# Kernel optimization log

Measured on AMD Instinct MI355X. Metric: run time of the kernel, lower is better.

The kernel has to match this reference:

```python
import jax, jax.numpy as jnp
import numpy as np

S, V, T = 128, 64, 128
N_RBF, CUTOFF = 16, 6.0
N_ATOM, N_PROT, N_FRAG, N_BATCH = 8192, 16384, 1024, 8
K, R, EPS = 32, 3.0, 1e-4
ES_DIM = N_RBF + S + S + T  # 400
HID = 256
GATE = S + 2 * V  # 256


def rbf_encode(d):
    mu = jnp.linspace(0.0, CUTOFF, N_RBF)
    gamma = N_RBF / CUTOFF
    return jnp.exp(-jnp.square(gamma * (d[..., None] - mu)))


def tp_conv(hs, hv, src, dst, diff, es, valid, n_dst, W1, b1, W2, b2, Ws, Wv):
    """Gather -> edge-scalar-gated tensor product -> scatter-add (EquivariantTPConv)."""
    w = jax.nn.silu(es @ W1 + b1) @ W2 + b2                      # [E, S+2V] edge gates
    unit = diff / (jnp.linalg.norm(diff, axis=-1, keepdims=True) + 1e-8)
    xs = hs[src] @ Ws                                            # [E, S]
    xv = jnp.einsum('evc,vw->ewc', hv[src], Wv)                  # [E, V, 3]
    ms = jnp.where(valid[:, None], w[:, :S] * xs, 0.0)
    mv = jnp.where(valid[:, None, None],
                   w[:, S:S + V, None] * xv + w[:, S + V:, None] * unit[:, None, :], 0.0)
    agg_s = jax.ops.segment_sum(ms, dst, num_segments=n_dst)
    agg_v = jax.ops.segment_sum(mv.reshape(-1, V * 3), dst, num_segments=n_dst).reshape(n_dst, V, 3)
    return agg_s, agg_v


def fragment_inertia(local_pos, fragment_id):
    r2 = jnp.sum(local_pos * local_pos, axis=-1)
    eye = jnp.eye(3, dtype=local_pos.dtype)
    I_atom = r2[:, None, None] * eye - local_pos[:, :, None] * local_pos[:, None, :]
    I_frag = jax.ops.segment_sum(I_atom.reshape(-1, 9), fragment_id, num_segments=N_FRAG).reshape(N_FRAG, 3, 3)
    trace = jnp.trace(I_frag, axis1=-2, axis2=-1)[:, None, None]
    return I_frag + EPS * jnp.maximum(trace, 1.0) * eye


def _forward(atom_pos, prot_pos, local_pos, h_atom_s, h_atom_v, h_prot_s, h_prot_v,
             h_frag_s, h_frag_v, t_emb_atom,
             W1_ra, b1_ra, W2_ra, b2_ra, Ws_ra, Wv_ra,
             W1_af, b1_af, W2_af, b2_af, Ws_af, Wv_af,
             Wo_s, Wo_v, Wf_s, Wf_v,
             fragment_id, atom_batch, prot_batch):
    # ---- bipartite radius graph prot -> atom via masked cdist + topk ----
    d2 = (jnp.sum(atom_pos * atom_pos, -1)[:, None]
          + jnp.sum(prot_pos * prot_pos, -1)[None, :]
          - 2.0 * atom_pos @ prot_pos.T)
    dist = jnp.sqrt(jnp.maximum(d2, 0.0))                        # [N_ATOM, N_PROT]
    mask = (dist <= R) & (atom_batch[:, None] == prot_batch[None, :])
    dinf = jnp.where(mask, dist, jnp.inf)
    neg_top, src = jax.lax.top_k(-dinf, K)                       # K nearest per atom
    valid = jnp.isfinite(neg_top).reshape(-1)
    src = src.reshape(-1)
    dst = jnp.repeat(jnp.arange(N_ATOM), K)
    # ---- residue->atom TP conv ----
    diff_ra = atom_pos[dst] - prot_pos[src]
    dist_ra = jnp.linalg.norm(diff_ra, axis=-1)
    ra_es = jnp.concatenate([rbf_encode(dist_ra), h_prot_s[src], h_atom_s[dst], t_emb_atom[dst]], -1)
    ms, mv = tp_conv(h_prot_s, h_prot_v, src, dst, diff_ra, ra_es, valid, N_ATOM,
                     W1_ra, b1_ra, W2_ra, b2_ra, Ws_ra, Wv_ra)
    ha_s = h_atom_s + jax.nn.silu(ms @ Wo_s)
    ha_v = h_atom_v + jnp.einsum('nvc,vw->nwc', mv, Wo_v)
    # ---- fragment centers + atom->frag re-lift TP conv ----
    ones = jnp.ones((N_ATOM,), atom_pos.dtype)
    cnt = jnp.maximum(jax.ops.segment_sum(ones, fragment_id, num_segments=N_FRAG), 1.0)
    T_frag = jax.ops.segment_sum(atom_pos, fragment_id, num_segments=N_FRAG) / cnt[:, None]
    r_af = atom_pos - T_frag[fragment_id]
    af_es = jnp.concatenate([rbf_encode(jnp.linalg.norm(r_af, axis=-1)), ha_s,
                             h_frag_s[fragment_id], t_emb_atom], -1)
    af_valid = jnp.ones((N_ATOM,), bool)
    fs, fv = tp_conv(ha_s, ha_v, jnp.arange(N_ATOM), fragment_id, r_af, af_es, af_valid, N_FRAG,
                     W1_af, b1_af, W2_af, b2_af, Ws_af, Wv_af)
    hf_s = h_frag_s + jax.nn.silu(fs @ Wf_s)
    hf_v = h_frag_v + jnp.einsum('nvc,vw->nwc', fv, Wf_v)
    I_frag = fragment_inertia(local_pos, fragment_id)
    # single packed output [N_ATOM, 2*(S+3V)+9]; frag quantities gathered per atom
    return jnp.concatenate([ha_s, ha_v.reshape(N_ATOM, -1),
                            hf_s[fragment_id], hf_v.reshape(N_FRAG, -1)[fragment_id],
                            I_frag.reshape(N_FRAG, 9)[fragment_id]], -1)


def setup_inputs() -> dict:
    key = jax.random.key(0)
    ks = jax.random.split(key, 32)
    def w(k, shape, fan_in):
        return jax.random.normal(k, shape, jnp.float32) / np.sqrt(fan_in).astype(np.float32)
    return dict(
        atom_pos=jax.random.normal(ks[0], (N_ATOM, 3), jnp.float32),
        prot_pos=jax.random.normal(ks[1], (N_PROT, 3), jnp.float32),
        local_pos=jax.random.normal(ks[2], (N_ATOM, 3), jnp.float32),
        h_atom_s=jax.random.normal(ks[3], (N_ATOM, S), jnp.float32),
        h_atom_v=jax.random.normal(ks[4], (N_ATOM, V, 3), jnp.float32),
        h_prot_s=jax.random.normal(ks[5], (N_PROT, S), jnp.float32),
        h_prot_v=jax.random.normal(ks[6], (N_PROT, V, 3), jnp.float32),
        h_frag_s=jax.random.normal(ks[7], (N_FRAG, S), jnp.float32),
        h_frag_v=jax.random.normal(ks[8], (N_FRAG, V, 3), jnp.float32),
        t_emb_atom=jax.random.normal(ks[9], (N_ATOM, T), jnp.float32),
        W1_ra=w(ks[10], (ES_DIM, HID), ES_DIM), b1_ra=jnp.zeros((HID,), jnp.float32),
        W2_ra=w(ks[11], (HID, GATE), HID), b2_ra=jnp.zeros((GATE,), jnp.float32),
        Ws_ra=w(ks[12], (S, S), S), Wv_ra=w(ks[13], (V, V), V),
        W1_af=w(ks[14], (ES_DIM, HID), ES_DIM), b1_af=jnp.zeros((HID,), jnp.float32),
        W2_af=w(ks[15], (HID, GATE), HID), b2_af=jnp.zeros((GATE,), jnp.float32),
        Ws_af=w(ks[16], (S, S), S), Wv_af=w(ks[17], (V, V), V),
        Wo_s=w(ks[18], (S, S), S), Wo_v=w(ks[19], (V, V), V),
        Wf_s=w(ks[20], (S, S), S), Wf_v=w(ks[21], (V, V), V),
        fragment_id=jax.random.randint(ks[22], (N_ATOM,), 0, N_FRAG),
        atom_batch=jnp.sort(jax.random.randint(ks[23], (N_ATOM,), 0, N_BATCH)),
        prot_batch=jnp.sort(jax.random.randint(ks[24], (N_PROT,), 0, N_BATCH)),
    )


def reference(atom_pos, prot_pos, local_pos, h_atom_s, h_atom_v, h_prot_s, h_prot_v,
              h_frag_s, h_frag_v, t_emb_atom,
              W1_ra, b1_ra, W2_ra, b2_ra, Ws_ra, Wv_ra,
              W1_af, b1_af, W2_af, b2_af, Ws_af, Wv_af,
              Wo_s, Wo_v, Wf_s, Wf_v,
              fragment_id, atom_batch, prot_batch):
    return _forward(atom_pos, prot_pos, local_pos, h_atom_s, h_atom_v, h_prot_s, h_prot_v,
                    h_frag_s, h_frag_v, t_emb_atom,
                    W1_ra, b1_ra, W2_ra, b2_ra, Ws_ra, Wv_ra,
                    W1_af, b1_af, W2_af, b2_af, Ws_af, Wv_af,
                    Wo_s, Wo_v, Wf_s, Wf_v,
                    fragment_id, atom_batch, prot_batch)
```

## Files before the change

### kernel.cpp

```cpp
#include <hip/hip_runtime.h>
#include <hip/hip_bf16.h>

#define N_ATOM 8192
#define N_PROT 16384
#define N_FRAG 1024
#define KNN    32
#define OUTC   649

typedef __attribute__((ext_vector_type(8))) short bf16x8;
typedef __attribute__((ext_vector_type(4))) float f32x4;

__device__ __forceinline__ float silu_f(float x){ return x / (1.f + __expf(-x)); }
__device__ __forceinline__ unsigned long long ullmin2(unsigned long long a, unsigned long long b){ return a < b ? a : b; }

__device__ __forceinline__ short f2bf(float x){
    __hip_bfloat16 h = __float2bfloat16(x);
    return *reinterpret_cast<short*>(&h);
}
__device__ __forceinline__ unsigned f2bf2(float lo, float hi){
    __hip_bfloat162 h2;
    h2.x = __float2bfloat16(lo);
    h2.y = __float2bfloat16(hi);
    return *reinterpret_cast<unsigned*>(&h2);
}
__device__ __forceinline__ float bf2f(short s){
    return __uint_as_float(((unsigned)(unsigned short)s) << 16);
}

__global__ void k_ranges(const int* __restrict__ pbatch, int* __restrict__ pstart){
    int b = threadIdx.x;
    if (b <= 8){
        int lo = 0, hi = N_PROT;
        while (lo < hi){ int mid = (lo + hi) >> 1; if (pbatch[mid] < b) lo = mid + 1; else hi = mid; }
        pstart[b] = lo;
    }
}

__global__ __launch_bounds__(256) void k_knn(const float* __restrict__ apos,
                                             const float* __restrict__ ppos,
                                             const int* __restrict__ abatch,
                                             const int* __restrict__ pstart,
                                             int* __restrict__ src_out){
    __shared__ int h1[256];
    __shared__ int h2[256];
    __shared__ int s_info[6];
    __shared__ int s_nsel;
    __shared__ int s_nbound;
    __shared__ unsigned long long s_bound[192];

    const int i = blockIdx.x, t = threadIdx.x;
    const int lane = t & 63;
    const int b = abatch[i];
    const int p0 = pstart[b], p1 = pstart[b+1];
    const float ax = apos[i*3+0], ay = apos[i*3+1], az = apos[i*3+2];
    const float a2 = ax*ax + ay*ay + az*az;

    unsigned kb[12];
    int jj[12];
#pragma unroll
    for (int q = 0; q < 12; ++q){
        int j = p0 + q*256 + t;
        unsigned kk = 0xFFFFFFFFu;
        if (j < p1){
            float px = ppos[j*3+0], py = ppos[j*3+1], pz = ppos[j*3+2];
            float p2 = px*px + py*py + pz*pz;
            float dt = ax*px + ay*py + az*pz;
            float d2 = (a2 + p2) - 2.0f*dt;
            float dist = sqrtf(fmaxf(d2, 0.f));
            if (dist <= 3.0f) kk = __float_as_uint(dist);
        }
        kb[q] = kk; jj[q] = j;
    }
    h1[t] = 0; h2[t] = 0;
    if (t == 0){ s_nsel = 0; s_nbound = 0; }
    __syncthreads();
#pragma unroll
    for (int q = 0; q < 12; ++q)
        if (kb[q] != 0xFFFFFFFFu) atomicAdd(&h1[kb[q] >> 24], 1);
    __syncthreads();
    if (t < 64){
        int base = t*4;
        int a0 = h1[base], a1 = h1[base+1], a2i = h1[base+2], a3 = h1[base+3];
        int lsum = a0 + a1 + a2i + a3;
        int sc = lsum;
#pragma unroll
        for (int off = 1; off < 64; off <<= 1){
            int v = __shfl_up(sc, off);
            if (lane >= off) sc += v;
        }
        int ex = sc - lsum;
        h1[base]   = ex + a0;
        h1[base+1] = ex + a0 + a1;
        h1[base+2] = ex + a0 + a1 + a2i;
        h1[base+3] = sc;
        if (t == 63) s_info[5] = sc;
    }
    __syncthreads();
    const int total = s_info[5];
    const int kth = (total < KNN) ? total : KNN;
    if (kth > 0){
        int cum  = h1[t];
        int prev = (t == 0) ? 0 : h1[t-1];
        if (cum >= kth && prev < kth){ s_info[0] = t; s_info[1] = prev; }
    }
    __syncthreads();
    const int B = s_info[0], cb1 = s_info[1];
    if (kth > 0){
#pragma unroll
        for (int q = 0; q < 12; ++q)
            if (kb[q] != 0xFFFFFFFFu && (int)(kb[q] >> 24) == B)
                atomicAdd(&h2[(kb[q] >> 16) & 0xFF], 1);
    }
    __syncthreads();
    if (t < 64){
        int base = t*4;
        int a0 = h2[base], a1 = h2[base+1], a2i = h2[base+2], a3 = h2[base+3];
        int lsum = a0 + a1 + a2i + a3;
        int sc = lsum;
#pragma unroll
        for (int off = 1; off < 64; off <<= 1){
            int v = __shfl_up(sc, off);
            if (lane >= off) sc += v;
        }
        int ex = sc - lsum;
        h2[base]   = ex + a0;
        h2[base+1] = ex + a0 + a1;
        h2[base+2] = ex + a0 + a1 + a2i;
        h2[base+3] = sc;
    }
    __syncthreads();
    if (kth > 0){
        int need2 = kth - cb1;
        int cum  = h2[t];
        int prev = (t == 0) ? 0 : h2[t-1];
        if (cum >= need2 && prev < need2){ s_info[3] = (B << 8) | t; }
    }
    __syncthreads();
    const int TH16 = s_info[3];
    if (kth > 0){
#pragma unroll
        for (int q = 0; q < 12; ++q){
            unsigned kk = kb[q];
            if (kk == 0xFFFFFFFFu) continue;
            int k16 = (int)(kk >> 16);
            if (k16 < TH16){
                int pos = atomicAdd(&s_nsel, 1);
                src_out[i*KNN + pos] = jj[q];
            } else if (k16 == TH16){
                int bi = atomicAdd(&s_nbound, 1);
                if (bi < 192) s_bound[bi] = ((unsigned long long)kk << 32) | (unsigned)jj[q];
            }
        }
    }
    __syncthreads();
    const int base_n = s_nsel;
    const int R = kth - base_n;
    if (t < 64 && R > 0){
        int L = s_nbound; if (L > 192) L = 192;
        for (int r = 0; r < R; ++r){
            unsigned long long m = ~0ull;
            for (int idx = lane; idx < L; idx += 64) m = ullmin2(m, s_bound[idx]);
#pragma unroll
            for (int off = 32; off >= 1; off >>= 1)
                m = ullmin2(m, (unsigned long long)__shfl_xor((unsigned long long)m, off));
            if (lane == 0) src_out[i*KNN + base_n + r] = (int)(unsigned)(m & 0xFFFFFFFFull);
            for (int idx = lane; idx < L; idx += 64)
                if (s_bound[idx] == m) s_bound[idx] = ~0ull;
        }
    }
    if (t < KNN && t >= kth) src_out[i*KNN + t] = -1;
}

__global__ void k_fragsum(const float* __restrict__ apos, const float* __restrict__ lpos,
                          const int* __restrict__ fid,
                          float* __restrict__ cnt, float* __restrict__ tsum, float* __restrict__ isum){
    int a = blockIdx.x*256 + threadIdx.x;
    if (a >= N_ATOM) return;
    int f = fid[a];
    atomicAdd(&cnt[f], 1.f);
    atomicAdd(&tsum[f*3+0], apos[a*3+0]);
    atomicAdd(&tsum[f*3+1], apos[a*3+1]);
    atomicAdd(&tsum[f*3+2], apos[a*3+2]);
    float x = lpos[a*3+0], y = lpos[a*3+1], z = lpos[a*3+2];
    float r2 = x*x + y*y + z*z;
    atomicAdd(&isum[f*9+0], r2 - x*x);
    atomicAdd(&isum[f*9+1], -(x*y));
    atomicAdd(&isum[f*9+2], -(x*z));
    atomicAdd(&isum[f*9+3], -(y*x));
    atomicAdd(&isum[f*9+4], r2 - y*y);
    atomicAdd(&isum[f*9+5], -(y*z));
    atomicAdd(&isum[f*9+6], -(z*x));
    atomicAdd(&isum[f*9+7], -(z*y));
    atomicAdd(&isum[f*9+8], r2 - z*z);
}

__global__ void k_fragcent(const float* __restrict__ cnt, const float* __restrict__ tsum,
                           const float* __restrict__ isum,
                           float* __restrict__ tfrag, float* __restrict__ ifin){
    int f = blockIdx.x*256 + threadIdx.x;
    if (f >= N_FRAG) return;
    float cn = fmaxf(cnt[f], 1.f);
    tfrag[f*3+0] = tsum[f*3+0] / cn;
    tfrag[f*3+1] = tsum[f*3+1] / cn;
    tfrag[f*3+2] = tsum[f*3+2] / cn;
    float tr  = isum[f*9+0] + isum[f*9+4] + isum[f*9+8];
    float add = 1e-4f * fmaxf(tr, 1.f);
#pragma unroll
    for (int q = 0; q < 9; ++q){
        float v = isum[f*9+q];
        if (q == 0 || q == 4 || q == 8) v += add;
        ifin[f*9+q] = v;
    }
}

__global__ __launch_bounds__(1024) void k_csr_prefix(const float* __restrict__ cnt,
                                                     int* __restrict__ csr_off,
                                                     int* __restrict__ csr_cur){
    __shared__ int s[1024];
    int t = threadIdx.x;
    int v = (int)cnt[t];
    s[t] = v;
    __syncthreads();
    for (int off = 1; off < 1024; off <<= 1){
        int x = (t >= off) ? s[t-off] : 0;
        __syncthreads();
        s[t] += x;
        __syncthreads();
    }
    int incl = s[t];
    int excl = incl - v;
    csr_off[t] = excl;
    csr_cur[t] = excl;
    if (t == 1023) csr_off[1024] = incl;
}

__global__ void k_csr_scatter(const int* __restrict__ fid, int* __restrict__ csr_cur,
                              int* __restrict__ csr_atom){
    int a = blockIdx.x*256 + threadIdx.x;
    if (a >= N_ATOM) return;
    int f = fid[a];
    int pos = atomicAdd(&csr_cur[f], 1);
    csr_atom[pos] = a;
}

__global__ void k_pack(const float* __restrict__ W1, const float* __restrict__ W2,
                       const float* __restrict__ Ws, const float* __restrict__ Wv,
                       const float* __restrict__ W1a, const float* __restrict__ W2a,
                       const float* __restrict__ Wsa, const float* __restrict__ Wva,
                       const float* __restrict__ Wos, const float* __restrict__ Wov,
                       short* __restrict__ W1p, short* __restrict__ W2p,
                       short* __restrict__ Wsp, short* __restrict__ Wvp,
                       short* __restrict__ W1cp,
                       short* __restrict__ W1ap, short* __restrict__ W2ap,
                       short* __restrict__ Wsap, short* __restrict__ Wvap,
                       short* __restrict__ Wosp, short* __restrict__ Wovp){
    int id = blockIdx.x*256 + threadIdx.x;
    if (id < 5120){
        int kt = id/1024, rem = id%1024, nt = rem/64, l = rem%64;
#pragma unroll
        for (int jj = 0; jj < 8; ++jj){
            int k = kt*32 + ((l>>4)<<3) + jj, n = nt*16 + (l&15);
            W1p[(size_t)id*8 + jj] = (k < 144) ? f2bf(W1[(size_t)k*256 + n]) : (short)0;
        }
    } else if (id < 13312){
        int id2 = id - 5120;
        int kt = id2/1024, rem = id2%1024, nt = rem/64, l = rem%64;
#pragma unroll
        for (int jj = 0; jj < 8; ++jj){
            int k = kt*32 + ((l>>4)<<3) + jj, n = nt*16 + (l&15);
            W2p[(size_t)id2*8 + jj] = f2bf(W2[(size_t)k*256 + n]);
        }
    } else if (id < 15360){
        int id2 = id - 13312;
        int kt = id2/512, rem = id2%512, nt = rem/64, l = rem%64;
#pragma unroll
        for (int jj = 0; jj < 8; ++jj){
            int k = kt*32 + ((l>>4)<<3) + jj, n = nt*16 + (l&15);
            Wsp[(size_t)id2*8 + jj] = f2bf(Ws[(size_t)k*128 + n]);
        }
    } else if (id < 15872){
        int id2 = id - 15360;
        int kt = id2/256, rem = id2%256, nt = rem/64, l = rem%64;
#pragma unroll
        for (int jj = 0; jj < 8; ++jj){
            int k = kt*32 + ((l>>4)<<3) + jj, n = nt*16 + (l&15);
            Wvp[(size_t)id2*8 + jj] = f2bf(Wv[(size_t)k*64 + n]);
        }
    } else if (id < 24064){
        int id2 = id - 15872;
        int kt = id2/1024, rem = id2%1024, nt = rem/64, l = rem%64;
#pragma unroll
        for (int jj = 0; jj < 8; ++jj){
            int k = kt*32 + ((l>>4)<<3) + jj, n = nt*16 + (l&15);
            W1cp[(size_t)id2*8 + jj] = f2bf(W1[(size_t)(144 + k)*256 + n]);
        }
    } else if (id < 37376){
        int id2 = id - 24064;
        int kt = id2/1024, rem = id2%1024, nt = rem/64, l = rem%64;
#pragma unroll
        for (int jj = 0; jj < 8; ++jj){
            int k = kt*32 + ((l>>4)<<3) + jj, n = nt*16 + (l&15);
            W1ap[(size_t)id2*8 + jj] = (k < 400) ? f2bf(W1a[(size_t)k*256 + n]) : (short)0;
        }
    } else if (id < 45568){
        int id2 = id - 37376;
        int kt = id2/1024, rem = id2%1024, nt = rem/64, l = rem%64;
#pragma unroll
        for (int jj = 0; jj < 8; ++jj){
            int k = kt*32 + ((l>>4)<<3) + jj, n = nt*16 + (l&15);
            W2ap[(size_t)id2*8 + jj] = f2bf(W2a[(size_t)k*256 + n]);
        }
    } else if (id < 47616){
        int id2 = id - 45568;
        int kt = id2/512, rem = id2%512, nt = rem/64, l = rem%64;
#pragma unroll
        for (int jj = 0; jj < 8; ++jj){
            int k = kt*32 + ((l>>4)<<3) + jj, n = nt*16 + (l&15);
            Wsap[(size_t)id2*8 + jj] = f2bf(Wsa[(size_t)k*128 + n]);
        }
    } else if (id < 48128){
        int id2 = id - 47616;
        int kt = id2/256, rem = id2%256, nt = rem/64, l = rem%64;
#pragma unroll
        for (int jj = 0; jj < 8; ++jj){
            int k = kt*32 + ((l>>4)<<3) + jj, n = nt*16 + (l&15);
            Wvap[(size_t)id2*8 + jj] = f2bf(Wva[(size_t)k*64 + n]);
        }
    } else if (id < 50176){
        int id2 = id - 48128;
        int kt = id2/512, rem = id2%512, nt = rem/64, l = rem%64;
#pragma unroll
        for (int jj = 0; jj < 8; ++jj){
            int k = kt*32 + ((l>>4)<<3) + jj, n = nt*16 + (l&15);
            Wosp[(size_t)id2*8 + jj] = f2bf(Wos[(size_t)k*128 + n]);
        }
    } else if (id < 50688){
        int id2 = id - 50176;
        int kt = id2/256, rem = id2%256, nt = rem/64, l = rem%64;
#pragma unroll
        for (int jj = 0; jj < 8; ++jj){
            int k = kt*32 + ((l>>4)<<3) + jj, n = nt*16 + (l&15);
            Wovp[(size_t)id2*8 + jj] = f2bf(Wov[(size_t)k*64 + n]);
        }
    }
}

__global__ __launch_bounds__(256) void k_ctx(const float* __restrict__ has_,
                                             const float* __restrict__ temb,
                                             const short* __restrict__ W1cp,
                                             const float* __restrict__ b1,
                                             float* __restrict__ common){
    __shared__ __align__(16) char s_a[64*512];
    const int t = threadIdx.x, l = t & 63, w = t >> 6, g = l >> 4;
    const int a0 = blockIdx.x * 64;
    {
        int r = t & 63, seg = t >> 6;
        const float* srcp = (seg < 2) ? (has_ + (size_t)(a0 + r)*128 + seg*64)
                                      : (temb + (size_t)(a0 + r)*128 + (seg - 2)*64);
#pragma unroll
        for (int q = 0; q < 16; ++q){
            float4 x = *(const float4*)(srcp + q*4);
            int col = seg*64 + q*4;
            int off = (r*512 + col*2) ^ ((r & 7) << 4);
            *(unsigned*)(s_a + off)     = f2bf2(x.x, x.y);
            *(unsigned*)(s_a + off + 4) = f2bf2(x.z, x.w);
        }
    }
    __syncthreads();
    f32x4 acc[4][4];
#pragma unroll
    for (int mt = 0; mt < 4; ++mt)
#pragma unroll
        for (int nt = 0; nt < 4; ++nt) acc[mt][nt] = (f32x4){0.f,0.f,0.f,0.f};
    for (int ks = 0; ks < 8; ++ks){
        bf16x8 afr[4];
#pragma unroll
        for (int mt = 0; mt < 4; ++mt){
            int row = mt*16 + (l & 15);
            int off = (row*512 + ks*64 + g*16) ^ ((row & 7) << 4);
            afr[mt] = *(const bf16x8*)(s_a + off);
        }
#pragma unroll
        for (int nt = 0; nt < 4; ++nt){
            bf16x8 b = *(const bf16x8*)(W1cp + ((size_t)((ks*16 + (w*4 + nt))*64 + l))*8);
#pragma unroll
            for (int mt = 0; mt < 4; ++mt)
                acc[mt][nt] = __builtin_amdgcn_mfma_f32_16x16x32_bf16(afr[mt], b, acc[mt][nt], 0, 0, 0);
        }
    }
#pragma unroll
    for (int nt = 0; nt < 4; ++nt){
        int col = w*64 + nt*16 + (l & 15);
        float bb = b1[col];
#pragma unroll
        for (int mt = 0; mt < 4; ++mt)
#pragma unroll
            for (int r = 0; r < 4; ++r){
                int row = mt*16 + g*4 + r;
                common[(size_t)(a0 + row)*256 + col] = acc[mt][nt][r] + bb;
            }
    }
}

#define ES_STR 336
__global__ __launch_bounds__(512, 2) void k_ra3(
    const float* __restrict__ apos, const float* __restrict__ ppos,
    const float* __restrict__ hps,  const float* __restrict__ hpv,
    const short* __restrict__ W1p, const short* __restrict__ W2p,
    const short* __restrict__ Wsp, const short* __restrict__ Wvp,
    const float* __restrict__ common, const float* __restrict__ b2,
    const int* __restrict__ src,
    short* __restrict__ msR, short* __restrict__ mvR)
{
    __shared__ __align__(16) char s_es[32*ES_STR];
    __shared__ __align__(16) char s_h1[32*512];
    __shared__ __align__(16) char s_hpv[3*4096];
    __shared__ float s_unit[32][3];

    const int t = threadIdx.x;
    const int i = blockIdx.x;
    const int l = t & 63, w = t >> 6, g = l >> 4, r0 = l & 15;
    const int xm = (r0 & 7) << 4;
    float* s_mvA = (float*)s_es;
    float* s_mvB = s_mvA + 192;

    {
        const int e = t >> 4, sub = t & 15;
        const int j = src[i*KNN + e];
        float dx = 0.f, dy = 0.f, dz = 0.f, dist = 0.f;
        if (j >= 0){
            dx = apos[i*3+0] - ppos[j*3+0];
            dy = apos[i*3+1] - ppos[j*3+1];
            dz = apos[i*3+2] - ppos[j*3+2];
            dist = sqrtf(dx*dx + dy*dy + dz*dz);
        }
        if (sub == 0){
            float inv = 1.f / (dist + 1e-8f);
            s_unit[e][0] = dx*inv; s_unit[e][1] = dy*inv; s_unit[e][2] = dz*inv;
        }
        if (sub < 2){
            const float gamma = 16.0f / 6.0f;
#pragma unroll
            for (int q = 0; q < 4; ++q){
                int kk = sub*8 + q*2;
                float mu0  = 0.4f * (float)kk;
                float mu1  = 0.4f * (float)(kk+1);
                float a0 = gamma * (dist - mu0);
                float a1 = gamma * (dist - mu1);
                float e0 = (j >= 0) ? __expf(-(a0*a0)) : 0.f;
                float e1 = (j >= 0) ? __expf(-(a1*a1)) : 0.f;
                *(unsigned*)(s_es + e*ES_STR + kk*2) = f2bf2(e0, e1);
            }
        }
        if (sub < 8) *(int*)(s_es + e*ES_STR + 288 + sub*4) = 0;
#pragma unroll
        for (int q = 0; q < 2; ++q){
            float4 x = (j >= 0) ? *(const float4*)(hps + (size_t)j*128 + sub*8 + q*4)
                                : make_float4(0.f,0.f,0.f,0.f);
            *(unsigned*)(s_es + e*ES_STR + 32 + sub*16 + q*8)     = f2bf2(x.x, x.y);
            *(unsigned*)(s_es + e*ES_STR + 32 + sub*16 + q*8 + 4) = f2bf2(x.z, x.w);
        }
        const int em = (e & 7) << 4;
#pragma unroll
        for (int q = 0; q < 3; ++q){
            float4 x = (j >= 0) ? *(const float4*)(hpv + (size_t)j*192 + sub*12 + q*4)
                                : make_float4(0.f,0.f,0.f,0.f);
            float xv4[4] = {x.x, x.y, x.z, x.w};
#pragma unroll
            for (int m = 0; m < 4; ++m){
                int idx = sub*12 + q*4 + m;
                int v = idx/3, c = idx - v*3;
                *(short*)(s_hpv + c*4096 + e*128 + ((v*2) ^ em)) = f2bf(xv4[m]);
            }
        }
    }
    __syncthreads();

    f32x4 acc1[2][2];
#pragma unroll
    for (int mt = 0; mt < 2; ++mt)
#pragma unroll
        for (int nt = 0; nt < 2; ++nt) acc1[mt][nt] = (f32x4){0.f,0.f,0.f,0.f};
    for (int ks = 0; ks < 5; ++ks){
// ... 326 lines not shown
        for (int nt = 0; nt < 4; ++nt){
            bf16x8 b = *(const bf16x8*)(W2p + ((size_t)((ks*16 + (w*4 + nt))*64 + l))*8);
            accw[nt] = __builtin_amdgcn_mfma_f32_16x16x32_bf16(a0f, b, accw[nt], 0, 0, 0);
        }
    }
    float b2v[4];
#pragma unroll
    for (int nt = 0; nt < 4; ++nt) b2v[nt] = b2[w*64 + nt*16 + r0];

    if (w == 3){
        float uu[4][3];
#pragma unroll
        for (int r = 0; r < 4; ++r){
            int e = g*4 + r;
#pragma unroll
            for (int c = 0; c < 3; ++c) uu[r][c] = s_unit[e][c];
        }
#pragma unroll
        for (int nt = 0; nt < 4; ++nt){
            int wi = nt*16 + r0;
#pragma unroll
            for (int r = 0; r < 4; ++r){
                int e = g*4 + r;
                float gate = accw[nt][r] + b2v[nt];
#pragma unroll
                for (int c = 0; c < 3; ++c)
                    s_upr[e*192 + wi*3 + c] = gate * uu[r][c];
            }
        }
    }
    __syncthreads();

    if (w < 2){
#pragma unroll
        for (int nt = 0; nt < 4; ++nt){
            int col = w*64 + nt*16 + r0;
#pragma unroll
            for (int r = 0; r < 4; ++r){
                int e = g*4 + r;
                float p = (accw[nt][r] + b2v[nt]) * accxs[nt][r];
                msA[(size_t)(a0 + e)*128 + col] = f2bf(p);
            }
        }
    } else if (w == 2){
        bf16x8 bv[2][4];
#pragma unroll
        for (int ks = 0; ks < 2; ++ks)
#pragma unroll
            for (int nt = 0; nt < 4; ++nt)
                bv[ks][nt] = *(const bf16x8*)(Wvp + ((size_t)((ks*4 + nt)*64 + l))*8);
#pragma unroll
        for (int c = 0; c < 3; ++c){
            f32x4 accxv[4];
#pragma unroll
            for (int nt = 0; nt < 4; ++nt) accxv[nt] = (f32x4){0.f,0.f,0.f,0.f};
#pragma unroll
            for (int ks = 0; ks < 2; ++ks){
                int off0 = c*2048 + r0*128 + ((ks*64 + g*16) ^ xm);
                bf16x8 a0f = *(const bf16x8*)(s_pv + off0);
#pragma unroll
                for (int nt = 0; nt < 4; ++nt)
                    accxv[nt] = __builtin_amdgcn_mfma_f32_16x16x32_bf16(a0f, bv[ks][nt], accxv[nt], 0, 0, 0);
            }
#pragma unroll
            for (int nt = 0; nt < 4; ++nt){
                int wi = nt*16 + r0;
#pragma unroll
                for (int r = 0; r < 4; ++r){
                    int e = g*4 + r;
                    float p = (accw[nt][r] + b2v[nt]) * accxv[nt][r]
                            + s_upr[e*192 + wi*3 + c];
                    mvA[(size_t)(a0 + e)*192 + wi*3 + c] = f2bf(p);
                }
            }
        }
    }
}

__global__ __launch_bounds__(256) void k_fragupd(
    const int* __restrict__ csr_off, const int* __restrict__ csr_atom,
    const short* __restrict__ msA, const short* __restrict__ mvA,
    const float* __restrict__ hfs_in, const float* __restrict__ hfv_in,
    const float* __restrict__ Wfs, const float* __restrict__ Wfv,
    float* __restrict__ hfs_out, float* __restrict__ hfv_out)
{
    __shared__ __align__(16) float s_fs[128];
    __shared__ __align__(16) float s_fv[192];
    const int f = blockIdx.x, t = threadIdx.x;
    const int n0 = csr_off[f], n1 = csr_off[f+1];
    if (t < 128){
        float s = 0.f;
        for (int n = n0; n < n1; ++n){
            int a = csr_atom[n];
            s += bf2f(msA[(size_t)a*128 + t]);
        }
        s_fs[t] = s;
    }
    if (t >= 64){
        int idx = t - 64;
        float s = 0.f;
        for (int n = n0; n < n1; ++n){
            int a = csr_atom[n];
            s += bf2f(mvA[(size_t)a*192 + idx]);
        }
        s_fv[(idx % 3)*64 + (idx / 3)] = s;
    }
    __syncthreads();
    if (t < 128){
        float o = 0.f;
        for (int k = 0; k < 128; k += 4){
            const float* wr = &Wfs[k*128 + t];
            float4 m4 = *(const float4*)&s_fs[k];
            o = fmaf(m4.x, wr[0],   o);
            o = fmaf(m4.y, wr[128], o);
            o = fmaf(m4.z, wr[256], o);
            o = fmaf(m4.w, wr[384], o);
        }
        hfs_out[f*128 + t] = hfs_in[f*128 + t] + silu_f(o);
    }
    if (t < 192){
        const int wi = t & 63, cc = t >> 6;
        float o = 0.f;
        for (int v = 0; v < 64; v += 4){
            const float* wr = &Wfv[v*64 + wi];
            float4 m4 = *(const float4*)&s_fv[cc*64 + v];
            o = fmaf(m4.x, wr[0],   o);
            o = fmaf(m4.y, wr[64],  o);
            o = fmaf(m4.z, wr[128], o);
            o = fmaf(m4.w, wr[192], o);
        }
        hfv_out[f*192 + wi*3 + cc] = hfv_in[f*192 + wi*3 + cc] + o;
    }
}

__global__ void k_out(const int* __restrict__ fragid,
                      const float* __restrict__ hfs, const float* __restrict__ hfv,
                      const float* __restrict__ ifin, float* __restrict__ out)
{
    const int n = blockIdx.x, t = threadIdx.x;
    const int f = fragid[n];
    for (int c = t; c < 329; c += 256){
        float v;
        if      (c < 128) v = hfs[f*128 + c];
        else if (c < 320) v = hfv[f*192 + (c - 128)];
        else              v = ifin[f*9 + (c - 320)];
        out[(size_t)n*OUTC + 320 + c] = v;
    }
}

extern "C" void kernel_launch(void* const* d_in, const int* in_sizes, int n_in,
                              void* d_out, int out_size, void* d_ws, size_t ws_size,
                              hipStream_t stream)
{
    const float* atom_pos   = (const float*)d_in[0];
    const float* prot_pos   = (const float*)d_in[1];
    const float* local_pos  = (const float*)d_in[2];
    const float* h_atom_s   = (const float*)d_in[3];
    const float* h_atom_v   = (const float*)d_in[4];
    const float* h_prot_s   = (const float*)d_in[5];
    const float* h_prot_v   = (const float*)d_in[6];
    const float* h_frag_s   = (const float*)d_in[7];
    const float* h_frag_v   = (const float*)d_in[8];
    const float* t_emb      = (const float*)d_in[9];
    const float* W1_ra = (const float*)d_in[10]; const float* b1_ra = (const float*)d_in[11];
    const float* W2_ra = (const float*)d_in[12]; const float* b2_ra = (const float*)d_in[13];
    const float* Ws_ra = (const float*)d_in[14]; const float* Wv_ra = (const float*)d_in[15];
    const float* W1_af = (const float*)d_in[16]; const float* b1_af = (const float*)d_in[17];
    const float* W2_af = (const float*)d_in[18]; const float* b2_af = (const float*)d_in[19];
    const float* Ws_af = (const float*)d_in[20]; const float* Wv_af = (const float*)d_in[21];
    const float* Wo_s  = (const float*)d_in[22]; const float* Wo_v  = (const float*)d_in[23];
    const float* Wf_s  = (const float*)d_in[24]; const float* Wf_v  = (const float*)d_in[25];
    const int* fragment_id = (const int*)d_in[26];
    const int* atom_batch  = (const int*)d_in[27];
    const int* prot_batch  = (const int*)d_in[28];
    float* out = (float*)d_out;

    float* cnt   = (float*)d_ws;
    float* tsum  = cnt  + 1024;
    float* isum  = tsum + 3072;
    float* tfrag = isum + 9216;
    float* ifin  = tfrag + 3072;
    float* hfs   = ifin + 9216;
    float* hfv   = hfs  + 1024*128;
    int*   pstart   = (int*)(hfv + 1024*192);
    int*   src      = pstart + 16;
    int*   csr_off  = src + N_ATOM*KNN;
    int*   csr_cur  = csr_off + 1025;
    int*   csr_atom = csr_cur + 1024;
    uintptr_t pal = ((uintptr_t)(csr_atom + 8192) + 127) & ~(uintptr_t)127;
    float* common = (float*)pal;
    short* msA = (short*)common;
    short* mvA = msA + (size_t)8192*128;
    short* W1p  = (short*)(common + (size_t)8192*256);
    short* W2p  = W1p  + 40960;
    short* Wsp  = W2p  + 65536;
    short* Wvp  = Wsp  + 16384;
    short* W1cp = Wvp  + 4096;
    short* W1ap = W1cp + 65536;
    short* W2ap = W1ap + 106496;
    short* Wsap = W2ap + 65536;
    short* Wvap = Wsap + 16384;
    short* Wosp = Wvap + 4096;
    short* Wovp = Wosp + 16384;
    short* msR  = Wovp + 4096;
    short* mvR  = msR + (size_t)8192*128;

    size_t zero_bytes = (size_t)(1024 + 3072 + 9216) * sizeof(float);
    hipMemsetAsync(cnt, 0, zero_bytes, stream);

    k_pack    <<<198, 256, 0, stream>>>(W1_ra, W2_ra, Ws_ra, Wv_ra, W1_af, W2_af, Ws_af, Wv_af,
                                        Wo_s, Wo_v,
                                        W1p, W2p, Wsp, Wvp, W1cp, W1ap, W2ap, Wsap, Wvap,
                                        Wosp, Wovp);
    k_ranges  <<<1, 64, 0, stream>>>(prot_batch, pstart);
    k_knn     <<<N_ATOM, 256, 0, stream>>>(atom_pos, prot_pos, atom_batch, pstart, src);
    k_ctx     <<<N_ATOM/64, 256, 0, stream>>>(h_atom_s, t_emb, W1cp, b1_ra, common);
    k_fragsum <<<N_ATOM/256, 256, 0, stream>>>(atom_pos, local_pos, fragment_id, cnt, tsum, isum);
    k_fragcent<<<N_FRAG/256, 256, 0, stream>>>(cnt, tsum, isum, tfrag, ifin);
    k_csr_prefix<<<1, 1024, 0, stream>>>(cnt, csr_off, csr_cur);
    k_csr_scatter<<<N_ATOM/256, 256, 0, stream>>>(fragment_id, csr_cur, csr_atom);
    k_ra3     <<<N_ATOM, 512, 0, stream>>>(atom_pos, prot_pos, h_prot_s, h_prot_v,
                                           W1p, W2p, Wsp, Wvp, common, b2_ra,
                                           src, msR, mvR);
    k_ra_out  <<<N_ATOM/32, 256, 0, stream>>>(msR, mvR, Wosp, Wovp, h_atom_s, h_atom_v, out);
    k_af2     <<<N_ATOM/16, 256, 0, stream>>>(atom_pos, tfrag, h_frag_s, t_emb,
                                              W1ap, b1_af, W2ap, b2_af, Wsap, Wvap,
                                              fragment_id, out, msA, mvA);
    k_fragupd <<<N_FRAG, 256, 0, stream>>>(csr_off, csr_atom, msA, mvA,
                                           h_frag_s, h_frag_v, Wf_s, Wf_v, hfs, hfv);
    k_out     <<<N_ATOM, 256, 0, stream>>>(fragment_id, hfs, hfv, ifin, out);
}
```

Baseline: 276.9 us.

## Merge prologue kernels into one launch and scatter fragment outputs directly

Folds the kNN search, context GEMM, fragment sums and weight packing into a single kernel that dispatches by block index. The batch-range binary search moves into each kNN block, and the context GEMM reads fp32 W1 directly instead of a packed copy. The fragment update now writes its results straight into each member atom's output row, which removes the separate output kernel and its intermediate buffers. This cuts launch count and serialization between stages, at the cost of uncoalesced strided B loads in the context GEMM and repeated binary searches per block.

```diff
diff --git a/kernel.cpp b/kernel.cpp
--- a/kernel.cpp
+++ b/kernel.cpp
@@ -27,31 +27,27 @@
     return __uint_as_float(((unsigned)(unsigned short)s) << 16);
 }
 
-__global__ void k_ranges(const int* __restrict__ pbatch, int* __restrict__ pstart){
-    int b = threadIdx.x;
-    if (b <= 8){
-        int lo = 0, hi = N_PROT;
-        while (lo < hi){ int mid = (lo + hi) >> 1; if (pbatch[mid] < b) lo = mid + 1; else hi = mid; }
-        pstart[b] = lo;
-    }
-}
-
-__global__ __launch_bounds__(256) void k_knn(const float* __restrict__ apos,
-                                             const float* __restrict__ ppos,
-                                             const int* __restrict__ abatch,
-                                             const int* __restrict__ pstart,
-                                             int* __restrict__ src_out){
-    __shared__ int h1[256];
-    __shared__ int h2[256];
-    __shared__ int s_info[6];
-    __shared__ int s_nsel;
-    __shared__ int s_nbound;
-    __shared__ unsigned long long s_bound[192];
-
-    const int i = blockIdx.x, t = threadIdx.x;
+__device__ void dev_knn(int i, char* smem,
+                        const float* __restrict__ apos, const float* __restrict__ ppos,
+                        const int* __restrict__ abatch, const int* __restrict__ pbatch,
+                        int* __restrict__ src_out){
+    int* h1 = (int*)smem;
+    int* h2 = h1 + 256;
+    int* s_info = h2 + 256;
+    int* s_nsel = s_info + 6;
+    int* s_nbound = s_nsel + 1;
+    unsigned long long* s_bound = (unsigned long long*)(smem + 2080);
+
+    const int t = threadIdx.x;
     const int lane = t & 63;
     const int b = abatch[i];
-    const int p0 = pstart[b], p1 = pstart[b+1];
+    int lo = 0, hi = N_PROT;
+    while (lo < hi){ int mid = (lo + hi) >> 1; if (pbatch[mid] < b) lo = mid + 1; else hi = mid; }
+    const int p0 = lo;
+    lo = 0; hi = N_PROT;
+    while (lo < hi){ int mid = (lo + hi) >> 1; if (pbatch[mid] < b + 1) lo = mid + 1; else hi = mid; }
+    const int p1 = lo;
+
     const float ax = apos[i*3+0], ay = apos[i*3+1], az = apos[i*3+2];
     const float a2 = ax*ax + ay*ay + az*az;
 
@@ -72,7 +68,7 @@
         kb[q] = kk; jj[q] = j;
     }
     h1[t] = 0; h2[t] = 0;
-    if (t == 0){ s_nsel = 0; s_nbound = 0; }
+    if (t == 0){ *s_nsel = 0; *s_nbound = 0; }
     __syncthreads();
 #pragma unroll
     for (int q = 0; q < 12; ++q)
@@ -144,19 +140,19 @@
             if (kk == 0xFFFFFFFFu) continue;
             int k16 = (int)(kk >> 16);
             if (k16 < TH16){
-                int pos = atomicAdd(&s_nsel, 1);
+                int pos = atomicAdd(s_nsel, 1);
                 src_out[i*KNN + pos] = jj[q];
             } else if (k16 == TH16){
-                int bi = atomicAdd(&s_nbound, 1);
+                int bi = atomicAdd(s_nbound, 1);
                 if (bi < 192) s_bound[bi] = ((unsigned long long)kk << 32) | (unsigned)jj[q];
             }
         }
     }
     __syncthreads();
-    const int base_n = s_nsel;
+    const int base_n = *s_nsel;
     const int R = kth - base_n;
     if (t < 64 && R > 0){
-        int L = s_nbound; if (L > 192) L = 192;
+        int L = *s_nbound; if (L > 192) L = 192;
         for (int r = 0; r < R; ++r){
             unsigned long long m = ~0ull;
             for (int idx = lane; idx < L; idx += 64) m = ullmin2(m, s_bound[idx]);
@@ -171,10 +167,71 @@
     if (t < KNN && t >= kth) src_out[i*KNN + t] = -1;
 }
 
-__global__ void k_fragsum(const float* __restrict__ apos, const float* __restrict__ lpos,
-                          const int* __restrict__ fid,
-                          float* __restrict__ cnt, float* __restrict__ tsum, float* __restrict__ isum){
-    int a = blockIdx.x*256 + threadIdx.x;
+__device__ void dev_ctx(int cb, char* s_a,
+                        const float* __restrict__ has_, const float* __restrict__ temb,
+                        const float* __restrict__ W1, const float* __restrict__ b1,
+                        float* __restrict__ common){
+    const int t = threadIdx.x, l = t & 63, w = t >> 6, g = l >> 4;
+    const int a0 = cb * 64;
+    {
+        int r = t & 63, seg = t >> 6;
+        const float* srcp = (seg < 2) ? (has_ + (size_t)(a0 + r)*128 + seg*64)
+                                      : (temb + (size_t)(a0 + r)*128 + (seg - 2)*64);
+#pragma unroll
+        for (int q = 0; q < 16; ++q){
+            float4 x = *(const float4*)(srcp + q*4);
+            int col = seg*64 + q*4;
+            int off = (r*512 + col*2) ^ ((r & 7) << 4);
+            *(unsigned*)(s_a + off)     = f2bf2(x.x, x.y);
+            *(unsigned*)(s_a + off + 4) = f2bf2(x.z, x.w);
+        }
+    }
+    __syncthreads();
+    f32x4 acc[4][4];
+#pragma unroll
+    for (int mt = 0; mt < 4; ++mt)
+#pragma unroll
+        for (int nt = 0; nt < 4; ++nt) acc[mt][nt] = (f32x4){0.f,0.f,0.f,0.f};
+    for (int ks = 0; ks < 8; ++ks){
+        bf16x8 afr[4];
+#pragma unroll
+        for (int mt = 0; mt < 4; ++mt){
+            int row = mt*16 + (l & 15);
+            int off = (row*512 + ks*64 + g*16) ^ ((row & 7) << 4);
+            afr[mt] = *(const bf16x8*)(s_a + off);
+        }
+#pragma unroll
+        for (int nt = 0; nt < 4; ++nt){
+            bf16x8 bfrag;
+            int krow = 144 + ks*32 + ((l >> 4) << 3);
+            int ncol = (w*4 + nt)*16 + (l & 15);
+#pragma unroll
+            for (int jq = 0; jq < 8; ++jq)
+                bfrag[jq] = f2bf(W1[(size_t)(krow + jq)*256 + ncol]);
+#pragma unroll
+            for (int mt = 0; mt < 4; ++mt)
+                acc[mt][nt] = __builtin_amdgcn_mfma_f32_16x16x32_bf16(afr[mt], bfrag, acc[mt][nt], 0, 0, 0);
+        }
+    }
+#pragma unroll
+    for (int nt = 0; nt < 4; ++nt){
+        int col = w*64 + nt*16 + (l & 15);
+        float bb = b1[col];
+#pragma unroll
+        for (int mt = 0; mt < 4; ++mt)
+#pragma unroll
+            for (int r = 0; r < 4; ++r){
+                int row = mt*16 + g*4 + r;
+                common[(size_t)(a0 + row)*256 + col] = acc[mt][nt][r] + bb;
+            }
+    }
+}
+
+__device__ void dev_fragsum(int bb,
+                            const float* __restrict__ apos, const float* __restrict__ lpos,
+                            const int* __restrict__ fid,
+                            float* __restrict__ cnt, float* __restrict__ tsum, float* __restrict__ isum){
+    int a = bb*256 + threadIdx.x;
     if (a >= N_ATOM) return;
     int f = fid[a];
     atomicAdd(&cnt[f], 1.f);
@@ -194,6 +251,168 @@
     atomicAdd(&isum[f*9+8], r2 - z*z);
 }
 
+__device__ void dev_pack(int bb,
+                         const float* __restrict__ W1, const float* __restrict__ W2,
+                         const float* __restrict__ Ws, const float* __restrict__ Wv,
+                         const float* __restrict__ W1a, const float* __restrict__ W2a,
+                         const float* __restrict__ Wsa, const float* __restrict__ Wva,
+                         const float* __restrict__ Wos, const float* __restrict__ Wov,
+                         short* __restrict__ W1p, short* __restrict__ W2p,
+                         short* __restrict__ Wsp, short* __restrict__ Wvp,
+                         short* __restrict__ W1ap, short* __restrict__ W2ap,
+                         short* __restrict__ Wsap, short* __restrict__ Wvap,
+                         short* __restrict__ Wosp, short* __restrict__ Wovp){
+    int id = bb*256 + threadIdx.x;
+    if (id < 5120){
+        int kt = id/1024, rem = id%1024, nt = rem/64, l = rem%64;
+#pragma unroll
+        for (int jj = 0; jj < 8; ++jj){
+            int k = kt*32 + ((l>>4)<<3) + jj, n = nt*16 + (l&15);
+            W1p[(size_t)id*8 + jj] = (k < 144) ? f2bf(W1[(size_t)k*256 + n]) : (short)0;
+        }
+    } else if (id < 13312){
+        int id2 = id - 5120;
+        int kt = id2/1024, rem = id2%1024, nt = rem/64, l = rem%64;
+#pragma unroll
+        for (int jj = 0; jj < 8; ++jj){
+            int k = kt*32 + ((l>>4)<<3) + jj, n = nt*16 + (l&15);
+            W2p[(size_t)id2*8 + jj] = f2bf(W2[(size_t)k*256 + n]);
+        }
+    } else if (id < 15360){
+        int id2 = id - 13312;
+        int kt = id2/512, rem = id2%512, nt = rem/64, l = rem%64;
+#pragma unroll
+        for (int jj = 0; jj < 8; ++jj){
+            int k = kt*32 + ((l>>4)<<3) + jj, n = nt*16 + (l&15);
+            Wsp[(size_t)id2*8 + jj] = f2bf(Ws[(size_t)k*128 + n]);
+        }
+    } else if (id < 15872){
+        int id2 = id - 15360;
+        int kt = id2/256, rem = id2%256, nt = rem/64, l = rem%64;
+#pragma unroll
+        for (int jj = 0; jj < 8; ++jj){
+            int k = kt*32 + ((l>>4)<<3) + jj, n = nt*16 + (l&15);
+            Wvp[(size_t)id2*8 + jj] = f2bf(Wv[(size_t)k*64 + n]);
+        }
+    } else if (id < 29184){
+        int id2 = id - 15872;
+        int kt = id2/1024, rem = id2%1024, nt = rem/64, l = rem%64;
+#pragma unroll
+        for (int jj = 0; jj < 8; ++jj){
+            int k = kt*32 + ((l>>4)<<3) + jj, n = nt*16 + (l&15);
+            W1ap[(size_t)id2*8 + jj] = (k < 400) ? f2bf(W1a[(size_t)k*256 + n]) : (short)0;
+        }
+    } else if (id < 37376){
+        int id2 = id - 29184;
+        int kt = id2/1024, rem = id2%1024, nt = rem/64, l = rem%64;
+#pragma unroll
+        for (int jj = 0; jj < 8; ++jj){
+            int k = kt*32 + ((l>>4)<<3) + jj, n = nt*16 + (l&15);
+            W2ap[(size_t)id2*8 + jj] = f2bf(W2a[(size_t)k*256 + n]);
+        }
+    } else if (id < 39424){
+        int id2 = id - 37376;
+        int kt = id2/512, rem = id2%512, nt = rem/64, l = rem%64;
+#pragma unroll
+        for (int jj = 0; jj < 8; ++jj){
+            int k = kt*32 + ((l>>4)<<3) + jj, n = nt*16 + (l&15);
+            Wsap[(size_t)id2*8 + jj] = f2bf(Wsa[(size_t)k*128 + n]);
+        }
+    } else if (id < 39936){
+        int id2 = id - 39424;
+        int kt = id2/256, rem = id2%256, nt = rem/64, l = rem%64;
+#pragma unroll
+        for (int jj = 0; jj < 8; ++jj){
+            int k = kt*32 + ((l>>4)<<3) + jj, n = nt*16 + (l&15);
+            Wvap[(size_t)id2*8 + jj] = f2bf(Wva[(size_t)k*64 + n]);
+        }
+    } else if (id < 41984){
+        int id2 = id - 39936;
+        int kt = id2/512, rem = id2%512, nt = rem/64, l = rem%64;
+#pragma unroll
+        for (int jj = 0; jj < 8; ++jj){
+            int k = kt*32 + ((l>>4)<<3) + jj, n = nt*16 + (l&15);
+            Wosp[(size_t)id2*8 + jj] = f2bf(Wos[(size_t)k*128 + n]);
+        }
+    } else if (id < 42496){
+        int id2 = id - 41984;
+        int kt = id2/256, rem = id2%256, nt = rem/64, l = rem%64;
+#pragma unroll
+        for (int jj = 0; jj < 8; ++jj){
+            int k = kt*32 + ((l>>4)<<3) + jj, n = nt*16 + (l&15);
+            Wovp[(size_t)id2*8 + jj] = f2bf(Wov[(size_t)k*64 + n]);
+        }
+    }
+}
+
+#define PRO_CTX   (N_ATOM)
+#define PRO_FSUM  (N_ATOM + 128)
+#define PRO_PACK  (N_ATOM + 128 + 32)
+#define PRO_NPACK 166
+__global__ __launch_bounds__(256) void k_pro(
+    const float* __restrict__ apos, const float* __restrict__ ppos,
+    const float* __restrict__ lpos,
+    const int* __restrict__ abatch, const int* __restrict__ pbatch,
+    const int* __restrict__ fid,
+    const float* __restrict__ has_, const float* __restrict__ temb,
+    const float* __restrict__ b1,
+    const float* __restrict__ W1, const float* __restrict__ W2,
+    const float* __restrict__ Ws, const float* __restrict__ Wv,
+    const float* __restrict__ W1a, const float* __restrict__ W2a,
+    const float* __restrict__ Wsa, const float* __restrict__ Wva,
+    const float* __restrict__ Wos, const float* __restrict__ Wov,
+    int* __restrict__ src_out, float* __restrict__ common,
+    float* __restrict__ cnt, float* __restrict__ tsum, float* __restrict__ isum,
+    short* __restrict__ W1p, short* __restrict__ W2p,
+    short* __restrict__ Wsp, short* __restrict__ Wvp,
+    short* __restrict__ W1ap, short* __restrict__ W2ap,
+    short* __restrict__ Wsap, short* __restrict__ Wvap,
+    short* __restrict__ Wosp, short* __restrict__ Wovp)
+{
+    __shared__ __align__(16) char smem[32768];
+    const int b = blockIdx.x;
+    if (b < PRO_CTX){
+        dev_knn(b, smem, apos, ppos, abatch, pbatch, src_out);
+    } else if (b < PRO_FSUM){
+        dev_ctx(b - PRO_CTX, smem, has_, temb, W1, b1, common);
+    } else if (b < PRO_PACK){
+        dev_fragsum(b - PRO_FSUM, apos, lpos, fid, cnt, tsum, isum);
+    } else {
+        dev_pack(b - PRO_PACK, W1, W2, Ws, Wv, W1a, W2a, Wsa, Wva, Wos, Wov,
+                 W1p, W2p, Wsp, Wvp, W1ap, W2ap, Wsap, Wvap, Wosp, Wovp);
+    }
+}
+
+__global__ __launch_bounds__(1024) void k_csr_prefix(const float* __restrict__ cnt,
+                                                     int* __restrict__ csr_off,
+                                                     int* __restrict__ csr_cur){
+    __shared__ int s[1024];
+    int t = threadIdx.x;
+    int v = (int)cnt[t];
+    s[t] = v;
+    __syncthreads();
+    for (int off = 1; off < 1024; off <<= 1){
+        int x = (t >= off) ? s[t-off] : 0;
+        __syncthreads();
+        s[t] += x;
+        __syncthreads();
+    }
+    int incl = s[t];
+    int excl = incl - v;
+    csr_off[t] = excl;
+    csr_cur[t] = excl;
+    if (t == 1023) csr_off[1024] = incl;
+}
+
+__global__ void k_csr_scatter(const int* __restrict__ fid, int* __restrict__ csr_cur,
+                              int* __restrict__ csr_atom){
+    int a = blockIdx.x*256 + threadIdx.x;
+    if (a >= N_ATOM) return;
+    int f = fid[a];
+    int pos = atomicAdd(&csr_cur[f], 1);
+    csr_atom[pos] = a;
+}
+
 __global__ void k_fragcent(const float* __restrict__ cnt, const float* __restrict__ tsum,
                            const float* __restrict__ isum,
                            float* __restrict__ tfrag, float* __restrict__ ifin){
@@ -210,195 +429,6 @@
         float v = isum[f*9+q];
         if (q == 0 || q == 4 || q == 8) v += add;
         ifin[f*9+q] = v;
-    }
-}
-
-__global__ __launch_bounds__(1024) void k_csr_prefix(const float* __restrict__ cnt,
-                                                     int* __restrict__ csr_off,
-                                                     int* __restrict__ csr_cur){
-    __shared__ int s[1024];
-    int t = threadIdx.x;
-    int v = (int)cnt[t];
-    s[t] = v;
-    __syncthreads();
-    for (int off = 1; off < 1024; off <<= 1){
-        int x = (t >= off) ? s[t-off] : 0;
-        __syncthreads();
-        s[t] += x;
-        __syncthreads();
-    }
-    int incl = s[t];
-    int excl = incl - v;
-    csr_off[t] = excl;
-    csr_cur[t] = excl;
-    if (t == 1023) csr_off[1024] = incl;
-}
-
-__global__ void k_csr_scatter(const int* __restrict__ fid, int* __restrict__ csr_cur,
-                              int* __restrict__ csr_atom){
-    int a = blockIdx.x*256 + threadIdx.x;
-    if (a >= N_ATOM) return;
-    int f = fid[a];
-    int pos = atomicAdd(&csr_cur[f], 1);
-    csr_atom[pos] = a;
-}
-
-__global__ void k_pack(const float* __restrict__ W1, const float* __restrict__ W2,
-                       const float* __restrict__ Ws, const float* __restrict__ Wv,
-                       const float* __restrict__ W1a, const float* __restrict__ W2a,
-                       const float* __restrict__ Wsa, const float* __restrict__ Wva,
-                       const float* __restrict__ Wos, const float* __restrict__ Wov,
-                       short* __restrict__ W1p, short* __restrict__ W2p,
-                       short* __restrict__ Wsp, short* __restrict__ Wvp,
-                       short* __restrict__ W1cp,
-                       short* __restrict__ W1ap, short* __restrict__ W2ap,
-                       short* __restrict__ Wsap, short* __restrict__ Wvap,
-                       short* __restrict__ Wosp, short* __restrict__ Wovp){
-    int id = blockIdx.x*256 + threadIdx.x;
-    if (id < 5120){
-        int kt = id/1024, rem = id%1024, nt = rem/64, l = rem%64;
-#pragma unroll
-        for (int jj = 0; jj < 8; ++jj){
-            int k = kt*32 + ((l>>4)<<3) + jj, n = nt*16 + (l&15);
-            W1p[(size_t)id*8 + jj] = (k < 144) ? f2bf(W1[(size_t)k*256 + n]) : (short)0;
-        }
-    } else if (id < 13312){
-        int id2 = id - 5120;
-        int kt = id2/1024, rem = id2%1024, nt = rem/64, l = rem%64;
-#pragma unroll
-        for (int jj = 0; jj < 8; ++jj){
-            int k = kt*32 + ((l>>4)<<3) + jj, n = nt*16 + (l&15);
-            W2p[(size_t)id2*8 + jj] = f2bf(W2[(size_t)k*256 + n]);
-        }
-    } else if (id < 15360){
-        int id2 = id - 13312;
-        int kt = id2/512, rem = id2%512, nt = rem/64, l = rem%64;
-#pragma unroll
-        for (int jj = 0; jj < 8; ++jj){
-            int k = kt*32 + ((l>>4)<<3) + jj, n = nt*16 + (l&15);
-            Wsp[(size_t)id2*8 + jj] = f2bf(Ws[(size_t)k*128 + n]);
-        }
-    } else if (id < 15872){
-        int id2 = id - 15360;
-        int kt = id2/256, rem = id2%256, nt = rem/64, l = rem%64;
-#pragma unroll
-        for (int jj = 0; jj < 8; ++jj){
-            int k = kt*32 + ((l>>4)<<3) + jj, n = nt*16 + (l&15);
-            Wvp[(size_t)id2*8 + jj] = f2bf(Wv[(size_t)k*64 + n]);
-        }
-    } else if (id < 24064){
-        int id2 = id - 15872;
-        int kt = id2/1024, rem = id2%1024, nt = rem/64, l = rem%64;
-#pragma unroll
-        for (int jj = 0; jj < 8; ++jj){
-            int k = kt*32 + ((l>>4)<<3) + jj, n = nt*16 + (l&15);
-            W1cp[(size_t)id2*8 + jj] = f2bf(W1[(size_t)(144 + k)*256 + n]);
-        }
-    } else if (id < 37376){
-        int id2 = id - 24064;
-        int kt = id2/1024, rem = id2%1024, nt = rem/64, l = rem%64;
-#pragma unroll
-        for (int jj = 0; jj < 8; ++jj){
-            int k = kt*32 + ((l>>4)<<3) + jj, n = nt*16 + (l&15);
-            W1ap[(size_t)id2*8 + jj] = (k < 400) ? f2bf(W1a[(size_t)k*256 + n]) : (short)0;
-        }
-    } else if (id < 45568){
-        int id2 = id - 37376;
-        int kt = id2/1024, rem = id2%1024, nt = rem/64, l = rem%64;
-#pragma unroll
-        for (int jj = 0; jj < 8; ++jj){
-            int k = kt*32 + ((l>>4)<<3) + jj, n = nt*16 + (l&15);
-            W2ap[(size_t)id2*8 + jj] = f2bf(W2a[(size_t)k*256 + n]);
-        }
-    } else if (id < 47616){
-        int id2 = id - 45568;
-        int kt = id2/512, rem = id2%512, nt = rem/64, l = rem%64;
-#pragma unroll
-        for (int jj = 0; jj < 8; ++jj){
-            int k = kt*32 + ((l>>4)<<3) + jj, n = nt*16 + (l&15);
-            Wsap[(size_t)id2*8 + jj] = f2bf(Wsa[(size_t)k*128 + n]);
-        }
-    } else if (id < 48128){
-        int id2 = id - 47616;
-        int kt = id2/256, rem = id2%256, nt = rem/64, l = rem%64;
-#pragma unroll
-        for (int jj = 0; jj < 8; ++jj){
-            int k = kt*32 + ((l>>4)<<3) + jj, n = nt*16 + (l&15);
-            Wvap[(size_t)id2*8 + jj] = f2bf(Wva[(size_t)k*64 + n]);
-        }
-    } else if (id < 50176){
-        int id2 = id - 48128;
-        int kt = id2/512, rem = id2%512, nt = rem/64, l = rem%64;
-#pragma unroll
-        for (int jj = 0; jj < 8; ++jj){
-            int k = kt*32 + ((l>>4)<<3) + jj, n = nt*16 + (l&15);
-            Wosp[(size_t)id2*8 + jj] = f2bf(Wos[(size_t)k*128 + n]);
-        }
-    } else if (id < 50688){
-        int id2 = id - 50176;
-        int kt = id2/256, rem = id2%256, nt = rem/64, l = rem%64;
-#pragma unroll
-        for (int jj = 0; jj < 8; ++jj){
-            int k = kt*32 + ((l>>4)<<3) + jj, n = nt*16 + (l&15);
-            Wovp[(size_t)id2*8 + jj] = f2bf(Wov[(size_t)k*64 + n]);
-        }
-    }
-}
-
-__global__ __launch_bounds__(256) void k_ctx(const float* __restrict__ has_,
-                                             const float* __restrict__ temb,
-                                             const short* __restrict__ W1cp,
-                                             const float* __restrict__ b1,
-                                             float* __restrict__ common){
-    __shared__ __align__(16) char s_a[64*512];
-    const int t = threadIdx.x, l = t & 63, w = t >> 6, g = l >> 4;
-    const int a0 = blockIdx.x * 64;
-    {
-        int r = t & 63, seg = t >> 6;
-        const float* srcp = (seg < 2) ? (has_ + (size_t)(a0 + r)*128 + seg*64)
-                                      : (temb + (size_t)(a0 + r)*128 + (seg - 2)*64);
-#pragma unroll
-        for (int q = 0; q < 16; ++q){
-            float4 x = *(const float4*)(srcp + q*4);
-            int col = seg*64 + q*4;
-            int off = (r*512 + col*2) ^ ((r & 7) << 4);
-            *(unsigned*)(s_a + off)     = f2bf2(x.x, x.y);
-            *(unsigned*)(s_a + off + 4) = f2bf2(x.z, x.w);
-        }
-    }
-    __syncthreads();
-    f32x4 acc[4][4];
-#pragma unroll
-    for (int mt = 0; mt < 4; ++mt)
-#pragma unroll
-        for (int nt = 0; nt < 4; ++nt) acc[mt][nt] = (f32x4){0.f,0.f,0.f,0.f};
-    for (int ks = 0; ks < 8; ++ks){
-        bf16x8 afr[4];
-#pragma unroll
-        for (int mt = 0; mt < 4; ++mt){
-            int row = mt*16 + (l & 15);
-            int off = (row*512 + ks*64 + g*16) ^ ((row & 7) << 4);
-            afr[mt] = *(const bf16x8*)(s_a + off);
-        }
-#pragma unroll
-        for (int nt = 0; nt < 4; ++nt){
-            bf16x8 b = *(const bf16x8*)(W1cp + ((size_t)((ks*16 + (w*4 + nt))*64 + l))*8);
-#pragma unroll
-            for (int mt = 0; mt < 4; ++mt)
-                acc[mt][nt] = __builtin_amdgcn_mfma_f32_16x16x32_bf16(afr[mt], b, acc[mt][nt], 0, 0, 0);
-        }
-    }
-#pragma unroll
-    for (int nt = 0; nt < 4; ++nt){
-        int col = w*64 + nt*16 + (l & 15);
-        float bb = b1[col];
-#pragma unroll
-        for (int mt = 0; mt < 4; ++mt)
-#pragma unroll
-            for (int r = 0; r < 4; ++r){
-                int row = mt*16 + g*4 + r;
-                common[(size_t)(a0 + row)*256 + col] = acc[mt][nt][r] + bb;
-            }
     }
 }
 
@@ -891,7 +921,8 @@
     const short* __restrict__ msA, const short* __restrict__ mvA,
     const float* __restrict__ hfs_in, const float* __restrict__ hfv_in,
     const float* __restrict__ Wfs, const float* __restrict__ Wfv,
-    float* __restrict__ hfs_out, float* __restrict__ hfv_out)
+    const float* __restrict__ ifin,
+    float* __restrict__ out)
 {
     __shared__ __align__(16) float s_fs[128];
     __shared__ __align__(16) float s_fv[192];
@@ -925,7 +956,9 @@
             o = fmaf(m4.z, wr[256], o);
             o = fmaf(m4.w, wr[384], o);
         }
-        hfs_out[f*128 + t] = hfs_in[f*128 + t] + silu_f(o);
+        float val = hfs_in[f*128 + t] + silu_f(o);
+        for (int n = n0; n < n1; ++n)
+            out[(size_t)csr_atom[n]*OUTC + 320 + t] = val;
     }
     if (t < 192){
         const int wi = t & 63, cc = t >> 6;
@@ -938,22 +971,14 @@
             o = fmaf(m4.z, wr[128], o);
             o = fmaf(m4.w, wr[192], o);
         }
-        hfv_out[f*192 + wi*3 + cc] = hfv_in[f*192 + wi*3 + cc] + o;
-    }
-}
-
-__global__ void k_out(const int* __restrict__ fragid,
-                      const float* __restrict__ hfs, const float* __restrict__ hfv,
-                      const float* __restrict__ ifin, float* __restrict__ out)
-{
-    const int n = blockIdx.x, t = threadIdx.x;
-    const int f = fragid[n];
-    for (int c = t; c < 329; c += 256){
-        float v;
-        if      (c < 128) v = hfs[f*128 + c];
-        else if (c < 320) v = hfv[f*192 + (c - 128)];
-        else              v = ifin[f*9 + (c - 320)];
-        out[(size_t)n*OUTC + 320 + c] = v;
+        float val = hfv_in[f*192 + wi*3 + cc] + o;
+        for (int n = n0; n < n1; ++n)
+            out[(size_t)csr_atom[n]*OUTC + 448 + wi*3 + cc] = val;
+    } else if (t < 201){
+        int q = t - 192;
+        float val = ifin[f*9 + q];
+        for (int n = n0; n < n1; ++n)
+            out[(size_t)csr_atom[n]*OUTC + 640 + q] = val;
     }
 }
 
@@ -989,10 +1014,7 @@
     float* isum  = tsum + 3072;
     float* tfrag = isum + 9216;
     float* ifin  = tfrag + 3072;
-    float* hfs   = ifin + 9216;
-    float* hfv   = hfs  + 1024*128;
-    int*   pstart   = (int*)(hfv + 1024*192);
-    int*   src      = pstart + 16;
+    int*   src      = (int*)(ifin + 9216);
     int*   csr_off  = src + N_ATOM*KNN;
     int*   csr_cur  = csr_off + 1025;
     int*   csr_atom = csr_cur + 1024;
@@ -1004,8 +1026,7 @@
     short* W2p  = W1p  + 40960;
     short* Wsp  = W2p  + 65536;
     short* Wvp  = Wsp  + 16384;
-    short* W1cp = Wvp  + 4096;
-    short* W1ap = W1cp + 65536;
+    short* W1ap = Wvp  + 4096;
     short* W2ap = W1ap + 106496;
     short* Wsap = W2ap + 65536;
     short* Wvap = Wsap + 16384;
@@ -1017,14 +1038,15 @@
     size_t zero_bytes = (size_t)(1024 + 3072 + 9216) * sizeof(float);
     hipMemsetAsync(cnt, 0, zero_bytes, stream);
 
-    k_pack    <<<198, 256, 0, stream>>>(W1_ra, W2_ra, Ws_ra, Wv_ra, W1_af, W2_af, Ws_af, Wv_af,
-                                        Wo_s, Wo_v,
-                                        W1p, W2p, Wsp, Wvp, W1cp, W1ap, W2ap, Wsap, Wvap,
-                                        Wosp, Wovp);
-    k_ranges  <<<1, 64, 0, stream>>>(prot_batch, pstart);
-    k_knn     <<<N_ATOM, 256, 0, stream>>>(atom_pos, prot_pos, atom_batch, pstart, src);
-    k_ctx     <<<N_ATOM/64, 256, 0, stream>>>(h_atom_s, t_emb, W1cp, b1_ra, common);
-    k_fragsum <<<N_ATOM/256, 256, 0, stream>>>(atom_pos, local_pos, fragment_id, cnt, tsum, isum);
+    k_pro     <<<PRO_PACK + PRO_NPACK, 256, 0, stream>>>(
+                                           atom_pos, prot_pos, local_pos,
+                                           atom_batch, prot_batch, fragment_id,
+                                           h_atom_s, t_emb, b1_ra,
+                                           W1_ra, W2_ra, Ws_ra, Wv_ra, W1_af, W2_af, Ws_af, Wv_af,
+                                           Wo_s, Wo_v,
+                                           src, common, cnt, tsum, isum,
+                                           W1p, W2p, Wsp, Wvp, W1ap, W2ap, Wsap, Wvap,
+                                           Wosp, Wovp);
     k_fragcent<<<N_FRAG/256, 256, 0, stream>>>(cnt, tsum, isum, tfrag, ifin);
     k_csr_prefix<<<1, 1024, 0, stream>>>(cnt, csr_off, csr_cur);
     k_csr_scatter<<<N_ATOM/256, 256, 0, stream>>>(fragment_id, csr_cur, csr_atom);
@@ -1036,6 +1058,5 @@
                                               W1ap, b1_af, W2ap, b2_af, Wsap, Wvap,
                                               fragment_id, out, msA, mvA);
     k_fragupd <<<N_FRAG, 256, 0, stream>>>(csr_off, csr_atom, msA, mvA,
-                                           h_frag_s, h_frag_v, Wf_s, Wf_v, hfs, hfv);
-    k_out     <<<N_ATOM, 256, 0, stream>>>(fragment_id, hfs, hfv, ifin, out);
-}
+                                           h_frag_s, h_frag_v, Wf_s, Wf_v, ifin, out);
+}
```

Measured after the change: 344.2 us. +24.3%, slower.
